# Optimization experiments

Hardware: AMD Instinct MI355X
Metric: run time of the kernel (lower is better)

Reference implementation:

```python
import jax, jax.numpy as jnp
import numpy as np

B, C1, C2, H, W = 4, 256, 256, 64, 64
K, S, P, D = 3, 1, 1, 1
KK = K * K
BN_EPS = 1e-5
MAX_OFF = float(K * D * 2)


def setup_inputs() -> dict:
    key = jax.random.key(0)
    ks = jax.random.split(key, 8)
    x = jax.random.normal(ks[0], (B, C1, H, W), jnp.float32)
    # offset/mask 3x3 conv (module zero-inits; small random values exercise bilinear sampling)
    w_om = jax.random.normal(ks[1], (3 * KK, C1, 3, 3), jnp.float32) * 0.01
    b_om = jax.random.normal(ks[2], (3 * KK,), jnp.float32) * 0.01
    # main DCN weight [C2, C1, K, K], Kaiming-ish scale
    w_dcn = jax.random.normal(ks[3], (C2, C1, K, K), jnp.float32) * np.float32(1.0 / np.sqrt(C1 * KK))
    bn_gamma = 1.0 + 0.1 * jax.random.normal(ks[4], (C2,), jnp.float32)
    bn_beta = 0.1 * jax.random.normal(ks[5], (C2,), jnp.float32)
    bn_mean = 0.1 * jax.random.normal(ks[6], (C2,), jnp.float32)
    bn_var = jax.random.uniform(ks[7], (C2,), jnp.float32, minval=0.5, maxval=1.5)
    return {"x": x, "w_om": w_om, "b_om": b_om, "w_dcn": w_dcn,
            "bn_gamma": bn_gamma, "bn_beta": bn_beta, "bn_mean": bn_mean, "bn_var": bn_var}


def _dcn_v2(x, w_om, b_om, w_dcn):
    # 1) offset/mask conv (3x3, stride S, 'same' pad)
    om = jax.lax.conv_general_dilated(
        x, w_om, window_strides=(S, S), padding=((1, 1), (1, 1)),
        dimension_numbers=("NCHW", "OIHW", "NCHW")) + b_om[None, :, None, None]
    Ho, Wo = om.shape[2], om.shape[3]
    # 2) clamp offsets, sigmoid mask (mmcv layout: per kernel pos [dy, dx] interleaved)
    off = jnp.clip(om[:, :2 * KK], -MAX_OFF, MAX_OFF).reshape(B, KK, 2, Ho, Wo)
    mask = jax.nn.sigmoid(om[:, 2 * KK:3 * KK])  # [B, KK, Ho, Wo]
    # 3) sampling positions: p = (h*S - P + i*D + dy, w*S - P + j*D + dx)
    ky, kx = jnp.meshgrid(jnp.arange(K), jnp.arange(K), indexing="ij")
    base_y = (ky.reshape(KK) * D)[:, None, None] + (jnp.arange(Ho) * S - P)[None, :, None]  # [KK,Ho,1]
    base_x = (kx.reshape(KK) * D)[:, None, None] + (jnp.arange(Wo) * S - P)[None, None, :]  # [KK,1,Wo]
    py = base_y.astype(x.dtype)[None] + off[:, :, 0]  # [B,KK,Ho,Wo]
    px = base_x.astype(x.dtype)[None] + off[:, :, 1]
    # 4) bilinear gather with zero outside boundaries (per-corner validity, mmcv semantics)
    y0 = jnp.floor(py); x0 = jnp.floor(px)
    ly = py - y0; lx = px - x0
    y0i = y0.astype(jnp.int32); x0i = x0.astype(jnp.int32)
    x_flat = x.reshape(B, C1, H * W)

    def gather(yi, xi):
        valid = ((yi >= 0) & (yi < H) & (xi >= 0) & (xi < W)).astype(x.dtype)
        idx = (jnp.clip(yi, 0, H - 1) * W + jnp.clip(xi, 0, W - 1)).reshape(B, 1, -1)
        g = jnp.take_along_axis(x_flat, idx, axis=2)
        return g.reshape(B, C1, KK, Ho, Wo), valid  # valid: [B,KK,Ho,Wo]

    v00, m00 = gather(y0i, x0i)
    v01, m01 = gather(y0i, x0i + 1)
    v10, m10 = gather(y0i + 1, x0i)
    v11, m11 = gather(y0i + 1, x0i + 1)
    w00 = ((1 - ly) * (1 - lx) * m00)[:, None]
    w01 = ((1 - ly) * lx * m01)[:, None]
    w10 = (ly * (1 - lx) * m10)[:, None]
    w11 = (ly * lx * m11)[:, None]
    col = (w00 * v00 + w01 * v01 + w10 * v10 + w11 * v11) * mask[:, None]  # [B,C1,KK,Ho,Wo]
    # 5) gather-conv accumulate: out[b,o,h,w] = sum_{c,k} W[o,c,k] * col[b,c,k,h,w]
    return jnp.einsum("ock,bckhw->bohw", w_dcn.reshape(C2, C1, KK), col)


def reference(x, w_om, b_om, w_dcn, bn_gamma, bn_beta, bn_mean, bn_var):
    out = _dcn_v2(x, w_om, b_om, w_dcn)
    inv = bn_gamma * jax.lax.rsqrt(bn_var + BN_EPS)
    out = out * inv[None, :, None, None] + (bn_beta - bn_mean * inv)[None, :, None, None]
    return jax.nn.silu(out)
```

## Files before the change

kernel.cpp:

```cpp
#include <hip/hip_runtime.h>
#include <math.h>

#define B_  4
#define C1_ 256
#define C2_ 256
#define H_  64
#define W_  64
#define HW_ 4096
#define KK_ 9

#define A_WA     0u
#define A_XT     1179648u
#define A_XPAIR  9568256u
#define A_MIDX   26345472u
#define A_MWGT   27525120u
#define A_WOM    29884416u
#define A_BN     30031872u

typedef short bf16x8 __attribute__((ext_vector_type(8)));
typedef float f32x4 __attribute__((ext_vector_type(4)));

__device__ __forceinline__ unsigned f2bfu(float f) {
  unsigned u = __builtin_bit_cast(unsigned, f);
  return (u + 0x7FFFu + ((u >> 16) & 1u)) >> 16;
}
__device__ __forceinline__ float bflo(unsigned g) {
  return __builtin_bit_cast(float, g << 16);
}
__device__ __forceinline__ float bfhi(unsigned g) {
  return __builtin_bit_cast(float, g & 0xFFFF0000u);
}
__device__ __forceinline__ void gload_lds16(const void* g, void* l) {
  __builtin_amdgcn_global_load_lds(
      (const __attribute__((address_space(1))) unsigned*)g,
      (__attribute__((address_space(3))) unsigned*)l, 16, 0, 0);
}

__device__ __forceinline__ void decode_bid512(int bid, int& b, int& h, int& ph) {
  const int xcd = bid & 7, slot = bid >> 3;
  b = xcd >> 1;
  h = (xcd & 1) * 32 + (slot >> 1);
  ph = slot & 1;
}

__device__ __forceinline__ void decode_bid256(int bid, int& b, int& h) {
  const int xcd = bid & 7, slot = bid >> 3;
  b = xcd >> 1;
  h = (xcd & 1) * 32 + slot;
}

__global__ __launch_bounds__(256) void prep(
    const float* __restrict__ x, const float* __restrict__ w_om,
    const float* __restrict__ w_dcn, const float* __restrict__ bn_gamma,
    const float* __restrict__ bn_beta, const float* __restrict__ bn_mean,
    const float* __restrict__ bn_var, unsigned short* __restrict__ xT,
    unsigned* __restrict__ xpair, unsigned short* __restrict__ Wa,
    unsigned short* __restrict__ Wom, float* __restrict__ bnbuf) {
  const int bid = blockIdx.x;
  const int tid = threadIdx.x;
  if (bid < 1024) {
    __shared__ unsigned short T[64][68];
    const int b = bid >> 8;
    const int rem = bid & 255;
    const int pos0 = (rem >> 2) * 64;
    const int c0 = (rem & 3) * 64;
    const int pl = tid & 63;
    const int ch = tid >> 6;
#pragma unroll
    for (int r = 0; r < 16; ++r) {
      const int cl = ch * 16 + r;
      const float v = x[((size_t)(b * C1_ + c0 + cl)) * HW_ + pos0 + pl];
      T[cl][pl] = (unsigned short)f2bfu(v);
    }
    if (tid < 64) {
      const int pe = min(pos0 + 64, HW_ - 1);
      T[tid][64] =
          (unsigned short)f2bfu(x[((size_t)(b * C1_ + c0 + tid)) * HW_ + pe]);
    }
    __syncthreads();
    unsigned short* dstT = xT + ((size_t)b * HW_ + pos0) * 256 + c0;
#pragma unroll
    for (int it = 0; it < 2; ++it) {
      const int q = it * 256 + tid;
      const int pp = q >> 3, cc = (q & 7) * 8;
      unsigned t0 = T[cc + 0][pp], t1 = T[cc + 1][pp], t2 = T[cc + 2][pp],
               t3 = T[cc + 3][pp], t4 = T[cc + 4][pp], t5 = T[cc + 5][pp],
               t6 = T[cc + 6][pp], t7 = T[cc + 7][pp];
      *(int4*)(dstT + (size_t)pp * 256 + cc) =
          make_int4(t0 | (t1 << 16), t2 | (t3 << 16), t4 | (t5 << 16),
                    t6 | (t7 << 16));
    }
    unsigned* dstP = xpair + ((size_t)b * HW_ + pos0) * 256 + c0;
#pragma unroll
    for (int it = 0; it < 4; ++it) {
      const int q = it * 256 + tid;
      const int pp = q >> 4;
      const int cc = (q & 15) * 4;
      unsigned p0 = (unsigned)T[cc + 0][pp] | ((unsigned)T[cc + 0][pp + 1] << 16);
      unsigned p1 = (unsigned)T[cc + 1][pp] | ((unsigned)T[cc + 1][pp + 1] << 16);
      unsigned p2 = (unsigned)T[cc + 2][pp] | ((unsigned)T[cc + 2][pp + 1] << 16);
      unsigned p3 = (unsigned)T[cc + 3][pp] | ((unsigned)T[cc + 3][pp + 1] << 16);
      *(uint4*)(dstP + (size_t)pp * 256 + cc) = make_uint4(p0, p1, p2, p3);
    }
  } else if (bid < 1024 + 2304) {
    const unsigned e = (bid - 1024) * 256 + tid;
    const unsigned kt = e >> 13, r2 = e & 8191;
    const unsigned kg = r2 >> 11, r3 = r2 & 2047, o = r3 >> 3, j = r3 & 7;
    const unsigned ck = kt * 32 + kg * 8 + j;
    const unsigned k = ck >> 8, c = ck & 255;
    Wa[e] = (unsigned short)f2bfu(w_dcn[((size_t)o * C1_ + c) * 9 + k]);
  } else {
    const int wb = bid - (1024 + 2304);
    if (wb == 0) {
      const int o = tid;
      float inv = bn_gamma[o] * rsqrtf(bn_var[o] + 1e-5f);
      bnbuf[o] = inv;
      bnbuf[256 + o] = bn_beta[o] - bn_mean[o] * inv;
    }
    const unsigned e = wb * 256 + tid;
    const unsigned kt = e >> 10, kg = (e >> 8) & 3, o = (e >> 3) & 31, j = e & 7;
    const unsigned ck = kt * 32 + kg * 8 + j;
    const unsigned k = ck >> 8, c = ck & 255;
    const float v = (o < 27) ? w_om[((size_t)o * C1_ + c) * 9 + k] : 0.f;
    Wom[e] = (unsigned short)f2bfu(v);
  }
}

__global__ __launch_bounds__(256) void om_gemm(
    const unsigned short* __restrict__ xT, const float* __restrict__ b_om,
    const unsigned short* __restrict__ Wom, int2* __restrict__ midx,
    float4* __restrict__ mwgt) {
  __shared__ short Ald[2][4096];
  __shared__ short Bld[2][4096];
  __shared__ float omld[32][33];

  int b, h, ph;
  decode_bid512(blockIdx.x, b, h, ph);
  const int tid = threadIdx.x;
  const int lane = tid & 63, wid = tid >> 6;
  const int wo = wid >> 1, wp = wid & 1;
  const int p = tid & 31;
  const int cr = tid >> 5;

  const unsigned short* xTb = xT + (size_t)b * HW_ * 256;

  f32x4 acc = (f32x4){0.f, 0.f, 0.f, 0.f};

  auto stageA = [&](int s, int buf) {
    const char* src = (const char*)(Wom + (size_t)s * 4096);
    gload_lds16(src + tid * 16, (char*)&Ald[buf][0] + tid * 16);
    gload_lds16(src + (256 + tid) * 16, (char*)&Ald[buf][0] + (256 + tid) * 16);
  };

  auto produce = [&](int s, int4& uA, int4& uB) {
    const int k = s >> 1;
    const int c0 = (s & 1) * 128 + cr * 16;
    const int hh = h - 1 + k / 3;
    const int ww = ph * 32 + p - 1 + k % 3;
    const bool v = ((unsigned)hh < (unsigned)H_) && ((unsigned)ww < (unsigned)W_);
    const unsigned short* pl = xTb + (size_t)(v ? hh * W_ + ww : 0) * 256 + c0;
    uA = v ? *(const int4*)pl : make_int4(0, 0, 0, 0);
    uB = v ? *(const int4*)(pl + 8) : make_int4(0, 0, 0, 0);
  };

  const int bslot = (cr * 2) * 256 + p * 8;

  auto compute = [&](int buf) {
    const int kg = lane >> 4, rr = lane & 15;
#pragma unroll
    for (int kh = 0; kh < 4; ++kh) {
      bf16x8 af = *(const bf16x8*)&Ald[buf][(kh * 4 + kg) * 256 + (wo * 16 + rr) * 8];
      bf16x8 bfr = *(const bf16x8*)&Bld[buf][(kh * 4 + kg) * 256 + (wp * 16 + rr) * 8];
      acc = __builtin_amdgcn_mfma_f32_16x16x32_bf16(af, bfr, acc, 0, 0, 0);
    }
  };

  {
    int4 uA, uB;
    produce(0, uA, uB);
    *(int4*)&Bld[0][bslot] = uA;
    *(int4*)&Bld[0][bslot + 256] = uB;
    stageA(0, 0);
  }
  __syncthreads();

  for (int s = 0; s < 18; ++s) {
    const int cur = s & 1, nxt = cur ^ 1;
    const bool pre = (s < 17);
    int4 uA, uB;
    if (pre) {
      produce(s + 1, uA, uB);
      stageA(s + 1, nxt);
    }
    compute(cur);
    if (pre) {
      *(int4*)&Bld[nxt][bslot] = uA;
      *(int4*)&Bld[nxt][bslot + 256] = uB;
    }
    __syncthreads();
  }

  {
    const int rr = lane & 15, rh = lane >> 4;
#pragma unroll
    for (int r = 0; r < 4; ++r) omld[wo * 16 + rh * 4 + r][wp * 16 + rr] = acc[r];
  }
  __syncthreads();

  if (tid < 32) {
    const int pc = tid;
    float a[27];
#pragma unroll
    for (int oc = 0; oc < 27; ++oc) a[oc] = omld[oc][pc] + b_om[oc];

    const int pcol = ph * 32 + pc;
#pragma unroll
    for (int k = 0; k < 9; ++k) {
      float dy = fminf(fmaxf(a[2 * k], -6.f), 6.f);
      float dx = fminf(fmaxf(a[2 * k + 1], -6.f), 6.f);
      float m = 1.f / (1.f + expf(-a[18 + k]));
      float py = (float)(h - 1 + k / 3) + dy;
      float px = (float)(pcol - 1 + k % 3) + dx;
      float y0f = floorf(py), x0f = floorf(px);
      float ly = py - y0f, lx = px - x0f;
      int y0 = (int)y0f, x0 = (int)x0f;
      int y1 = y0 + 1, x1 = x0 + 1;
      const bool vy0 = ((unsigned)y0 < (unsigned)H_);
      const bool vy1 = ((unsigned)y1 < (unsigned)H_);
      const bool vx0 = ((unsigned)x0 < (unsigned)W_);
      const bool vx1 = ((unsigned)x1 < (unsigned)W_);
      int y0c = min(max(y0, 0), H_ - 1), y1c = min(max(y1, 0), H_ - 1);
      int x0c = min(max(x0, 0), W_ - 1), x1c = min(max(x1, 0), W_ - 1);
      const int xbc = min(max(x0, 0), W_ - 2);
      float wx0 = 0.f, wx1 = 0.f;
      if (vx0) { if (x0c == xbc) wx0 += 1.f - lx; else wx1 += 1.f - lx; }
      if (vx1) { if (x1c == xbc) wx0 += lx; else wx1 += lx; }
      const float wy0 = vy0 ? (1.f - ly) : 0.f;
      const float wy1 = vy1 ? ly : 0.f;
      const size_t e = ((size_t)b * KK_ + k) * HW_ + h * W_ + pcol;
      midx[e] = make_int2(y0c * W_ + xbc, y1c * W_ + xbc);
      mwgt[e] = make_float4(m * wy0 * wx0, m * wy0 * wx1, m * wy1 * wx0,
                            m * wy1 * wx1);
    }
  }
}

__global__ __launch_bounds__(1024, 4) void dcn_fused(
    const unsigned short* __restrict__ Wa, const unsigned* __restrict__ xpair,
    const int2* __restrict__ midxg, const float4* __restrict__ mwgtg,
    const float* __restrict__ bnbuf, float* __restrict__ out) {
  __shared__ short Ald[2][16384];
  __shared__ short Bld[2][4096];

  int b, h;
  decode_bid256(blockIdx.x, b, h);
  const int tid = threadIdx.x;
  const int lane = tid & 63, wid = tid >> 6;
  const int wo = wid >> 1, wp = wid & 1;
  const int col = tid >> 4;
  const int q = tid & 15;

  const unsigned* xpb = xpair + (size_t)b * HW_ * 256;
  const int pg = h * W_ + col;

  int2 miR[9];
  float4 mwR[9];
#pragma unroll
  for (int k = 0; k < 9; ++k) {
    miR[k] = midxg[(size_t)b * KK_ * HW_ + (size_t)k * HW_ + pg];
    mwR[k] = mwgtg[(size_t)b * KK_ * HW_ + (size_t)k * HW_ + pg];
  }

  f32x4 acc[2][2];
#pragma unroll
  for (int i = 0; i < 2; ++i)
#pragma unroll
    for (int j = 0; j < 2; ++j) acc[i][j] = (f32x4){0.f, 0.f, 0.f, 0.f};

  auto stageA = [&](int s, int buf) {
    const char* src = (const char*)(Wa + (size_t)s * 16384);
#pragma unroll
    for (int r = 0; r < 2; ++r) {
      const int chunk = r * 1024 + tid;
      gload_lds16(src + chunk * 16, (char*)&Ald[buf][0] + chunk * 16);
    }
  };

  auto issue = [&](int s, uint4& ga, uint4& gb) {
    const int k = s >> 2;
    const int c0 = (s & 3) * 64 + q * 4;
    ga = *(const uint4*)(xpb + (size_t)miR[k].x * 256 + c0);
    gb = *(const uint4*)(xpb + (size_t)miR[k].y * 256 + c0);
  };

  auto pack = [&](int s, const uint4 ga, const uint4 gb, int2& pk) {
    const float4 mw = mwR[s >> 2];
    const unsigned a[4] = {ga.x, ga.y, ga.z, ga.w};
    const unsigned g[4] = {gb.x, gb.y, gb.z, gb.w};
    unsigned bf[4];
#pragma unroll
    for (int i = 0; i < 4; ++i) {
      float v = mw.x * bflo(a[i]) + mw.y * bfhi(a[i]) + mw.z * bflo(g[i]) +
                mw.w * bfhi(g[i]);
      bf[i] = f2bfu(v);
    }
    pk.x = bf[0] | (bf[1] << 16);
    pk.y = bf[2] | (bf[3] << 16);
  };

  const int wpage = q >> 1;
  const int wcol = col ^ wpage;
  const int bslot = (q >> 3) * 2048 + ((q >> 1) & 3) * 512 + wcol * 8 + (q & 1) * 4;

  auto compute = [&](int buf) {
    const int kg = lane >> 4, rr = lane & 15;
    bf16x8 af[2][2], bfr[2][2];
#pragma unroll
    for (int kh = 0; kh < 2; ++kh) {
      const int page = kh * 4 + kg;
#pragma unroll
      for (int fm = 0; fm < 2; ++fm)
        af[fm][kh] = *(const bf16x8*)&Ald[buf][kh * 8192 + kg * 2048 +
                                              (wo * 32 + fm * 16 + rr) * 8];
#pragma unroll
      for (int fn = 0; fn < 2; ++fn) {
        const int rc = (wp * 32 + fn * 16 + rr) ^ page;
        bfr[fn][kh] = *(const bf16x8*)&Bld[buf][kh * 2048 + kg * 512 + rc * 8];
      }
    }
#pragma unroll
    for (int kh = 0; kh < 2; ++kh)
#pragma unroll
      for (int fm = 0; fm < 2; ++fm)
#pragma unroll
        for (int fn = 0; fn < 2; ++fn)
          acc[fm][fn] = __builtin_amdgcn_mfma_f32_16x16x32_bf16(
              af[fm][kh], bfr[fn][kh], acc[fm][fn], 0, 0, 0);
  };

  uint4 ga, gb;
  {
    int2 pk;
    issue(0, ga, gb);
    pack(0, ga, gb, pk);
    *(int2*)&Bld[0][bslot] = pk;
    stageA(0, 0);
  }
  __syncthreads();

#pragma unroll
  for (int s = 0; s < 36; ++s) {
    const int cur = s & 1, nxt = cur ^ 1;
    if (s < 35) {
      issue(s + 1, ga, gb);
      stageA(s + 1, nxt);
    }
    compute(cur);
    if (s < 35) {
      int2 pk;
      pack(s + 1, ga, gb, pk);
      *(int2*)&Bld[nxt][bslot] = pk;
    }
    __syncthreads();
  }

  const float* bninv = bnbuf;
  const float* bnbb = bnbuf + 256;
  const int rr = lane & 15, rh = lane >> 4;
#pragma unroll
  for (int fm = 0; fm < 2; ++fm) {
#pragma unroll
    for (int r = 0; r < 4; ++r) {
      const int o = wo * 32 + fm * 16 + rh * 4 + r;
      const float inv = bninv[o], bb = bnbb[o];
#pragma unroll
      for (int fn = 0; fn < 2; ++fn) {
        float t = acc[fm][fn][r] * inv + bb;
        float sv = t / (1.f + expf(-t));
        out[(size_t)(b * C2_ + o) * HW_ + h * W_ + wp * 32 + fn * 16 + rr] = sv;
      }
    }
  }
}

extern "C" void kernel_launch(void* const* d_in, const int* in_sizes, int n_in,
                              void* d_out, int out_size, void* d_ws,
                              size_t ws_size, hipStream_t stream) {
  const float* x = (const float*)d_in[0];
  const float* w_om = (const float*)d_in[1];
  const float* b_om = (const float*)d_in[2];
  const float* w_dcn = (const float*)d_in[3];
  const float* bn_gamma = (const float*)d_in[4];
  const float* bn_beta = (const float*)d_in[5];
  const float* bn_mean = (const float*)d_in[6];
  const float* bn_var = (const float*)d_in[7];
  float* out = (float*)d_out;
  char* wsb = (char*)d_ws;

  unsigned short* Wa = (unsigned short*)(wsb + A_WA);
  unsigned short* xT = (unsigned short*)(wsb + A_XT);
  unsigned* xpair = (unsigned*)(wsb + A_XPAIR);
  int2* midx = (int2*)(wsb + A_MIDX);
  float4* mwgt = (float4*)(wsb + A_MWGT);
  unsigned short* Wom = (unsigned short*)(wsb + A_WOM);
  float* bnbuf = (float*)(wsb + A_BN);

  prep<<<1024 + 2304 + 288, 256, 0, stream>>>(x, w_om, w_dcn, bn_gamma,
                                              bn_beta, bn_mean, bn_var, xT,
                                              xpair, Wa, Wom, bnbuf);
  om_gemm<<<512, 256, 0, stream>>>(xT, b_om, Wom, midx, mwgt);
  dcn_fused<<<256, 1024, 0, stream>>>(Wa, xpair, midx, mwgt, bnbuf, out);
}
```

Baseline: 74.98 us.

## Deepen gather prefetch to two stages with explicit waitcnt and barriers

```diff
diff --git a/kernel.cpp b/kernel.cpp
--- a/kernel.cpp
+++ b/kernel.cpp
@@ -308,9 +308,8 @@
     pk.y = bf[2] | (bf[3] << 16);
   };
 
-  const int wpage = q >> 1;
-  const int wcol = col ^ wpage;
-  const int bslot = (q >> 3) * 2048 + ((q >> 1) & 3) * 512 + wcol * 8 + (q & 1) * 4;
+  const int bslot =
+      (q >> 3) * 2048 + ((q >> 1) & 3) * 512 + (col ^ (q >> 1)) * 8 + (q & 1) * 4;
 
   auto compute = [&](int buf) {
     const int kg = lane >> 4, rr = lane & 15;
@@ -338,31 +337,47 @@
               af[fm][kh], bfr[fn][kh], acc[fm][fn], 0, 0, 0);
   };
 
-  uint4 ga, gb;
+  uint4 ga_e, gb_e, ga_o, gb_o;
+
+  issue(0, ga_e, gb_e);
   {
     int2 pk;
-    issue(0, ga, gb);
-    pack(0, ga, gb, pk);
+    pack(0, ga_e, gb_e, pk);
     *(int2*)&Bld[0][bslot] = pk;
-    stageA(0, 0);
-  }
-  __syncthreads();
-
-#pragma unroll
-  for (int s = 0; s < 36; ++s) {
-    const int cur = s & 1, nxt = cur ^ 1;
-    if (s < 35) {
-      issue(s + 1, ga, gb);
-      stageA(s + 1, nxt);
-    }
-    compute(cur);
-    if (s < 35) {
-      int2 pk;
-      pack(s + 1, ga, gb, pk);
-      *(int2*)&Bld[nxt][bslot] = pk;
-    }
-    __syncthreads();
-  }
+  }
+  stageA(0, 0);
+  issue(1, ga_o, gb_o);
+  asm volatile("s_waitcnt vmcnt(2) lgkmcnt(0)" ::: "memory");
+  __builtin_amdgcn_s_barrier();
+  __builtin_amdgcn_sched_barrier(0);
+
+#define STEP(S, GAP, GBP, GAN, GBN)                                  \
+  {                                                                  \
+    if ((S) + 1 < 36) {                                              \
+      int2 pk;                                                       \
+      pack((S) + 1, GAP, GBP, pk);                                   \
+      *(int2*)&Bld[((S) + 1) & 1][bslot] = pk;                       \
+      stageA((S) + 1, ((S) + 1) & 1);                                \
+    }                                                                \
+    if ((S) + 2 < 36) issue((S) + 2, GAN, GBN);                      \
+    compute((S) & 1);                                                \
+    if ((S) + 1 < 36) {                                              \
+      if ((S) + 2 < 36) {                                            \
+        asm volatile("s_waitcnt vmcnt(2) lgkmcnt(0)" ::: "memory");  \
+      } else {                                                       \
+        asm volatile("s_waitcnt vmcnt(0) lgkmcnt(0)" ::: "memory");  \
+      }                                                              \
+      __builtin_amdgcn_s_barrier();                                  \
+      __builtin_amdgcn_sched_barrier(0);                             \
+    }                                                                \
+  }
+
+#pragma unroll
+  for (int sb = 0; sb < 36; sb += 2) {
+    STEP(sb, ga_o, gb_o, ga_e, gb_e);
+    STEP(sb + 1, ga_e, gb_e, ga_o, gb_o);
+  }
+#undef STEP
 
   const float* bninv = bnbuf;
   const float* bnbb = bnbuf + 256;
```

After: 73.16 us. -2.4%, faster.

## Halve dcn_fused block to 512 threads with 64x32 per-wave output tiles

Applied to the files above, without the earlier changes.

```diff
diff --git a/kernel.cpp b/kernel.cpp
--- a/kernel.cpp
+++ b/kernel.cpp
@@ -245,7 +245,7 @@
   }
 }
 
-__global__ __launch_bounds__(1024, 4) void dcn_fused(
+__global__ __launch_bounds__(512) void dcn_fused(
     const unsigned short* __restrict__ Wa, const unsigned* __restrict__ xpair,
     const int2* __restrict__ midxg, const float4* __restrict__ mwgtg,
     const float* __restrict__ bnbuf, float* __restrict__ out) {
@@ -257,8 +257,8 @@
   const int tid = threadIdx.x;
   const int lane = tid & 63, wid = tid >> 6;
   const int wo = wid >> 1, wp = wid & 1;
-  const int col = tid >> 4;
-  const int q = tid & 15;
+  const int col = tid >> 3;
+  const int q = tid & 7;
 
   const unsigned* xpb = xpair + (size_t)b * HW_ * 256;
   const int pg = h * W_ + col;
@@ -271,57 +271,62 @@
     mwR[k] = mwgtg[(size_t)b * KK_ * HW_ + (size_t)k * HW_ + pg];
   }
 
-  f32x4 acc[2][2];
-#pragma unroll
-  for (int i = 0; i < 2; ++i)
+  f32x4 acc[4][2];
+#pragma unroll
+  for (int i = 0; i < 4; ++i)
 #pragma unroll
     for (int j = 0; j < 2; ++j) acc[i][j] = (f32x4){0.f, 0.f, 0.f, 0.f};
 
   auto stageA = [&](int s, int buf) {
     const char* src = (const char*)(Wa + (size_t)s * 16384);
 #pragma unroll
-    for (int r = 0; r < 2; ++r) {
-      const int chunk = r * 1024 + tid;
+    for (int r = 0; r < 4; ++r) {
+      const int chunk = r * 512 + tid;
       gload_lds16(src + chunk * 16, (char*)&Ald[buf][0] + chunk * 16);
     }
   };
 
-  auto issue = [&](int s, uint4& ga, uint4& gb) {
+  auto issue = [&](int s, uint4& ga0, uint4& ga1, uint4& gb0, uint4& gb1) {
     const int k = s >> 2;
-    const int c0 = (s & 3) * 64 + q * 4;
-    ga = *(const uint4*)(xpb + (size_t)miR[k].x * 256 + c0);
-    gb = *(const uint4*)(xpb + (size_t)miR[k].y * 256 + c0);
-  };
-
-  auto pack = [&](int s, const uint4 ga, const uint4 gb, int2& pk) {
+    const int c0 = (s & 3) * 64 + q * 8;
+    const unsigned* r0 = xpb + (size_t)miR[k].x * 256 + c0;
+    const unsigned* r1 = xpb + (size_t)miR[k].y * 256 + c0;
+    ga0 = *(const uint4*)r0;
+    ga1 = *(const uint4*)(r0 + 4);
+    gb0 = *(const uint4*)r1;
+    gb1 = *(const uint4*)(r1 + 4);
+  };
+
+  auto pack = [&](int s, const uint4 ga0, const uint4 ga1, const uint4 gb0,
+                  const uint4 gb1, int4& pk) {
     const float4 mw = mwR[s >> 2];
-    const unsigned a[4] = {ga.x, ga.y, ga.z, ga.w};
-    const unsigned g[4] = {gb.x, gb.y, gb.z, gb.w};
-    unsigned bf[4];
-#pragma unroll
-    for (int i = 0; i < 4; ++i) {
+    const unsigned a[8] = {ga0.x, ga0.y, ga0.z, ga0.w, ga1.x, ga1.y, ga1.z, ga1.w};
+    const unsigned g[8] = {gb0.x, gb0.y, gb0.z, gb0.w, gb1.x, gb1.y, gb1.z, gb1.w};
+    unsigned bf[8];
+#pragma unroll
+    for (int i = 0; i < 8; ++i) {
       float v = mw.x * bflo(a[i]) + mw.y * bfhi(a[i]) + mw.z * bflo(g[i]) +
                 mw.w * bfhi(g[i]);
       bf[i] = f2bfu(v);
     }
     pk.x = bf[0] | (bf[1] << 16);
     pk.y = bf[2] | (bf[3] << 16);
-  };
-
-  const int wpage = q >> 1;
-  const int wcol = col ^ wpage;
-  const int bslot = (q >> 3) * 2048 + ((q >> 1) & 3) * 512 + wcol * 8 + (q & 1) * 4;
+    pk.z = bf[4] | (bf[5] << 16);
+    pk.w = bf[6] | (bf[7] << 16);
+  };
+
+  const int bslot = (q >> 2) * 2048 + (q & 3) * 512 + (col ^ q) * 8;
 
   auto compute = [&](int buf) {
     const int kg = lane >> 4, rr = lane & 15;
-    bf16x8 af[2][2], bfr[2][2];
+    bf16x8 af[4][2], bfr[2][2];
 #pragma unroll
     for (int kh = 0; kh < 2; ++kh) {
       const int page = kh * 4 + kg;
 #pragma unroll
-      for (int fm = 0; fm < 2; ++fm)
+      for (int fm = 0; fm < 4; ++fm)
         af[fm][kh] = *(const bf16x8*)&Ald[buf][kh * 8192 + kg * 2048 +
-                                              (wo * 32 + fm * 16 + rr) * 8];
+                                              (wo * 64 + fm * 16 + rr) * 8];
 #pragma unroll
       for (int fn = 0; fn < 2; ++fn) {
         const int rc = (wp * 32 + fn * 16 + rr) ^ page;
@@ -331,19 +336,20 @@
 #pragma unroll
     for (int kh = 0; kh < 2; ++kh)
 #pragma unroll
-      for (int fm = 0; fm < 2; ++fm)
+      for (int fm = 0; fm < 4; ++fm)
 #pragma unroll
         for (int fn = 0; fn < 2; ++fn)
           acc[fm][fn] = __builtin_amdgcn_mfma_f32_16x16x32_bf16(
               af[fm][kh], bfr[fn][kh], acc[fm][fn], 0, 0, 0);
   };
 
-  uint4 ga, gb;
+  uint4 ga0, ga1, gb0, gb1;
+
   {
-    int2 pk;
-    issue(0, ga, gb);
-    pack(0, ga, gb, pk);
-    *(int2*)&Bld[0][bslot] = pk;
+    int4 pk;
+    issue(0, ga0, ga1, gb0, gb1);
+    pack(0, ga0, ga1, gb0, gb1, pk);
+    *(int4*)&Bld[0][bslot] = pk;
     stageA(0, 0);
   }
   __syncthreads();
@@ -352,14 +358,14 @@
   for (int s = 0; s < 36; ++s) {
     const int cur = s & 1, nxt = cur ^ 1;
     if (s < 35) {
-      issue(s + 1, ga, gb);
+      issue(s + 1, ga0, ga1, gb0, gb1);
       stageA(s + 1, nxt);
     }
     compute(cur);
     if (s < 35) {
-      int2 pk;
-      pack(s + 1, ga, gb, pk);
-      *(int2*)&Bld[nxt][bslot] = pk;
+      int4 pk;
+      pack(s + 1, ga0, ga1, gb0, gb1, pk);
+      *(int4*)&Bld[nxt][bslot] = pk;
     }
     __syncthreads();
   }
@@ -368,10 +374,10 @@
   const float* bnbb = bnbuf + 256;
   const int rr = lane & 15, rh = lane >> 4;
 #pragma unroll
-  for (int fm = 0; fm < 2; ++fm) {
+  for (int fm = 0; fm < 4; ++fm) {
 #pragma unroll
     for (int r = 0; r < 4; ++r) {
-      const int o = wo * 32 + fm * 16 + rh * 4 + r;
+      const int o = wo * 64 + fm * 16 + rh * 4 + r;
       const float inv = bninv[o], bb = bnbb[o];
 #pragma unroll
       for (int fn = 0; fn < 2; ++fn) {
@@ -409,5 +415,5 @@
                                               bn_beta, bn_mean, bn_var, xT,
                                               xpair, Wa, Wom, bnbuf);
   om_gemm<<<512, 256, 0, stream>>>(xT, b_om, Wom, midx, mwgt);
-  dcn_fused<<<256, 1024, 0, stream>>>(Wa, xpair, midx, mwgt, bnbuf, out);
-}
+  dcn_fused<<<256, 512, 0, stream>>>(Wa, xpair, midx, mwgt, bnbuf, out);
+}
```

Measured after the change: 80.27 us. 1.07x slower.
